# Optimization experiments

Hardware: AMD Instinct MI355X
Metric: run time of the kernel (lower is better)

The kernel has to match this reference:

```python
import jax, jax.numpy as jnp
import numpy as np
from jax import lax

S, B, IN, H, L = 256, 8192, 1, 32, 2


def setup_inputs() -> dict:
    key = jax.random.key(0)
    ks = jax.random.split(key, 12)
    s = 1.0 / np.sqrt(H)
    return {
        "x": jax.random.normal(ks[0], (S, B, IN), dtype=jnp.float32),
        "h": jax.random.normal(ks[1], (L, B, H), dtype=jnp.float32),
        "W_ih0": jax.random.uniform(ks[2], (3 * H, IN), jnp.float32, -s, s),
        "W_hh0": jax.random.uniform(ks[3], (3 * H, H), jnp.float32, -s, s),
        "b_ih0": jax.random.uniform(ks[4], (3 * H,), jnp.float32, -s, s),
        "b_hh0": jax.random.uniform(ks[5], (3 * H,), jnp.float32, -s, s),
        "W_ih1": jax.random.uniform(ks[6], (3 * H, H), jnp.float32, -s, s),
        "W_hh1": jax.random.uniform(ks[7], (3 * H, H), jnp.float32, -s, s),
        "b_ih1": jax.random.uniform(ks[8], (3 * H,), jnp.float32, -s, s),
        "b_hh1": jax.random.uniform(ks[9], (3 * H,), jnp.float32, -s, s),
        "W_out": jax.random.uniform(ks[10], (1, H), jnp.float32, -s, s),
        "b_out": jax.random.uniform(ks[11], (1,), jnp.float32, -s, s),
    }


def _gru_layer(x_seq, h0, W_ih, W_hh, b_ih, b_hh):
    # x_seq: (S, B, D_in), h0: (B, H). PyTorch GRU gate math.
    def step(h, x_t):
        gi = x_t @ W_ih.T + b_ih            # (B, 3H)
        gh = h @ W_hh.T + b_hh              # (B, 3H)
        i_r, i_z, i_n = jnp.split(gi, 3, axis=-1)
        h_r, h_z, h_n = jnp.split(gh, 3, axis=-1)
        r = jax.nn.sigmoid(i_r + h_r)
        z = jax.nn.sigmoid(i_z + h_z)
        n = jnp.tanh(i_n + r * h_n)
        h_new = (1.0 - z) * n + z * h
        return h_new, h_new

    h_last, out = lax.scan(step, h0, x_seq)
    return out, h_last


def reference(x, h, W_ih0, W_hh0, b_ih0, b_hh0, W_ih1, W_hh1, b_ih1, b_hh1, W_out, b_out):
    out0, hl0 = _gru_layer(x, h[0], W_ih0, W_hh0, b_ih0, b_hh0)
    out1, hl1 = _gru_layer(out0, h[1], W_ih1, W_hh1, b_ih1, b_hh1)
    # per-timestep Linear loop == one batched matmul over (S, B, H)
    y = out1 @ W_out.T + b_out              # (S, B, 1)
    h_state = jnp.stack([hl0, hl1], axis=0)  # (L, B, H)
    return (y, h_state)
```

## Files before the change

kernel.cpp:

```cpp
#include <hip/hip_runtime.h>


#define S_LEN 256
#define B_SZ  8192
#define H_SZ  32
#define RS    40

typedef __attribute__((ext_vector_type(8))) short short8;
typedef __attribute__((ext_vector_type(4))) float f32x4;

#define MFMA(a, b, c) __builtin_amdgcn_mfma_f32_16x16x32_bf16(a, b, c, 0, 0, 0)

__device__ __forceinline__ unsigned short bf_rne1(float f) {
    union { float f; unsigned u; } x; x.f = f;
    unsigned u = x.u + 0x7fffu + ((x.u >> 16) & 1u);
    return (unsigned short)(u >> 16);
}

#if __has_builtin(__builtin_amdgcn_cvt_pk_bf16_f32)
typedef __bf16 bf16x2 __attribute__((ext_vector_type(2)));
__device__ __forceinline__ unsigned pk2(float a, float b) {
    union { bf16x2 v; unsigned u; } c;
    c.v = __builtin_amdgcn_cvt_pk_bf16_f32(a, b);
    return c.u;
}
#else
__device__ __forceinline__ unsigned pk2(float a, float b) {
    return (unsigned)bf_rne1(a) | ((unsigned)bf_rne1(b) << 16);
}
#endif

union Frag8 { short8 s8; unsigned u[4]; };

__device__ __forceinline__ uint2 gru_combine(const f32x4& Dr, const f32x4& Dz,
                                             const f32x4& Dn, const f32x4& Dxn,
                                             float* hm) {
    float v4[4];
#pragma unroll
    for (int r = 0; r < 4; ++r) {
        const float Er = __builtin_amdgcn_exp2f(Dr[r]);
        const float rg = __builtin_amdgcn_rcpf(1.0f + Er);
        const float X  = __builtin_amdgcn_exp2f(fmaf(rg, Dn[r], Dxn[r]));
        const float Ez = __builtin_amdgcn_exp2f(Dz[r]);
        const float Nx = 1.0f + X;
        const float Nz = 1.0f + Ez;
        const float P  = Nx * Nz;
        float num = fmaf(-2.0f, Ez, P);
        num = fmaf(hm[r], Nx, num);
        const float v = num * __builtin_amdgcn_rcpf(P);
        hm[r] = v - 1.0f;
        v4[r] = v;
    }
    return make_uint2(pk2(v4[0], v4[1]), pk2(v4[2], v4[3]));
}

__global__ __launch_bounds__(256) void gru_xm(
    const float* __restrict__ x,
    const float* __restrict__ h_in,
    const float* __restrict__ W_ih0,
    const float* __restrict__ W_hh0,
    const float* __restrict__ b_ih0,
    const float* __restrict__ b_hh0,
    const float* __restrict__ W_ih1,
    const float* __restrict__ W_hh1,
    const float* __restrict__ b_ih1,
    const float* __restrict__ b_hh1,
    const float* __restrict__ W_out,
    const float* __restrict__ b_out,
    float* __restrict__ out)
{
    __shared__ __align__(16) unsigned short sh0[2][16 * RS];
    __shared__ __align__(16) unsigned short sh1[2][16 * RS];
    __shared__ __align__(16) float sx[(S_LEN + 1) * 16];
    __shared__ __align__(16) float sy[S_LEN * 16];

    const int tid  = threadIdx.x;
    const int w    = tid >> 6;
    const int lane = tid & 63;
    const int n    = lane & 15;
    const int q    = lane >> 4;
    const int base = blockIdx.x * 16;
    const int bn   = base + n;
    const int wl   = w & 1;

    for (int s = tid; s < S_LEN * 4; s += 256) {
        const int t = s >> 2, c = s & 3;
        *(float4*)&sx[t * 16 + c * 4] = *(const float4*)&x[t * B_SZ + base + c * 4];
    }

    const float SRZ = -1.4426950408889634f;
    const float SN  =  2.8853900817779268f;

    short8 A_h[3], A_i[3];
    f32x4  C_h[3], C_i3;
    short8 Awo = {0, 0, 0, 0, 0, 0, 0, 0};
    short8 Bx  = {0, 0, 0, 0, 0, 0, 0, 0};
    float  hm[4];

    if (w < 2) {
#pragma unroll
        for (int t = 0; t < 3; ++t) {
            const float sc = (t < 2) ? SRZ : SN;
            const int row = 32 * t + 16 * wl + n;
#pragma unroll
            for (int e = 0; e < 8; ++e)
                A_h[t][e] = (short)bf_rne1(W_hh0[row * H_SZ + q * 8 + e] * sc);
#pragma unroll
            for (int e = 0; e < 8; ++e)
                A_i[t][e] = (q == 0 && e == 0)
                            ? (short)bf_rne1(W_ih0[row] * sc) : (short)0;
#pragma unroll
            for (int r = 0; r < 4; ++r) {
                const int g = 32 * t + 16 * wl + 4 * q + r;
                C_h[t][r] = (t < 2) ? SRZ * (b_ih0[g] + b_hh0[g])
                                    : SN * b_hh0[g];
                if (t == 2) C_i3[r] = SN * b_ih0[g];
            }
        }
#pragma unroll
        for (int r = 0; r < 4; ++r)
            hm[r] = h_in[bn * H_SZ + 16 * wl + 4 * q + r] - 1.0f;
    } else {
#pragma unroll
        for (int t = 0; t < 3; ++t) {
            const float sc = (t < 2) ? SRZ : SN;
            const int row = 32 * t + 16 * wl + n;
#pragma unroll
            for (int e = 0; e < 8; ++e) {
                A_h[t][e] = (short)bf_rne1(W_hh1[row * H_SZ + q * 8 + e] * sc);
                A_i[t][e] = (short)bf_rne1(W_ih1[row * H_SZ + q * 8 + e] * sc);
            }
#pragma unroll
            for (int r = 0; r < 4; ++r) {
                const int g = 32 * t + 16 * wl + 4 * q + r;
                C_h[t][r] = (t < 2) ? SRZ * (b_ih1[g] + b_hh1[g])
                                    : SN * b_hh1[g];
                if (t == 2) C_i3[r] = SN * b_ih1[g];
            }
        }
#pragma unroll
        for (int r = 0; r < 4; ++r)
            hm[r] = h_in[B_SZ * H_SZ + bn * H_SZ + 16 * wl + 4 * q + r] - 1.0f;
#pragma unroll
        for (int e = 0; e < 8; ++e)
            Awo[e] = (n == 0) ? (short)bf_rne1(W_out[q * 8 + e]) : (short)0;
    }
    const f32x4 Z4 = {0.f, 0.f, 0.f, 0.f};
    const float bout = b_out[0];

    short8 B0, B1;
    {
        const float* hsrc = h_in + (size_t)(w >= 2) * B_SZ * H_SZ + bn * H_SZ + q * 8;
        Frag8 f;
        const float4 a = *(const float4*)&hsrc[0];
        const float4 b = *(const float4*)&hsrc[4];
        f.u[0] = pk2(a.x, a.y); f.u[1] = pk2(a.z, a.w);
        f.u[2] = pk2(b.x, b.y); f.u[3] = pk2(b.z, b.w);
        if (w < 2) B0 = f.s8; else B1 = f.s8;
    }

    const int wroff = n * RS + 16 * wl + 4 * q;
    const int rdoff = n * RS + 8 * q;

    __syncthreads();
    float xcur = sx[n];
    if (w < 2) __builtin_amdgcn_s_setprio(1);

    if (w < 2) {
        Frag8 bxu; bxu.s8 = Bx; bxu.u[0] = pk2(xcur, xcur); Bx = bxu.s8;
        f32x4 Dr = MFMA(A_h[0], B0, C_h[0]);  Dr = MFMA(A_i[0], Bx, Dr);
        f32x4 Dz = MFMA(A_h[1], B0, C_h[1]);  Dz = MFMA(A_i[1], Bx, Dz);
        f32x4 Dn = MFMA(A_h[2], B0, C_h[2]);
        f32x4 Dxn = MFMA(A_i[2], Bx, C_i3);
        *(uint2*)&sh0[0][wroff] = gru_combine(Dr, Dz, Dn, Dxn, hm);
        xcur = sx[16 + n];
    }
    __syncthreads();
    B0 = *(const short8*)&sh0[0][rdoff];

#pragma unroll 2
    for (int i = 1; i < S_LEN; ++i) {
        const int buf = i & 1;
        if (w < 2) {
            Frag8 bxu; bxu.s8 = Bx; bxu.u[0] = pk2(xcur, xcur); Bx = bxu.s8;
            f32x4 Dr = MFMA(A_h[0], B0, C_h[0]);  Dr = MFMA(A_i[0], Bx, Dr);
            f32x4 Dz = MFMA(A_h[1], B0, C_h[1]);  Dz = MFMA(A_i[1], Bx, Dz);
            f32x4 Dn = MFMA(A_h[2], B0, C_h[2]);
            f32x4 Dxn = MFMA(A_i[2], Bx, C_i3);
            *(uint2*)&sh0[buf][wroff] = gru_combine(Dr, Dz, Dn, Dxn, hm);
            xcur = sx[(i + 1) * 16 + n];
        } else {
            f32x4 Gr = MFMA(A_h[0], B1, C_h[0]);  Gr = MFMA(A_i[0], B0, Gr);
            f32x4 Gz = MFMA(A_h[1], B1, C_h[1]);  Gz = MFMA(A_i[1], B0, Gz);
            f32x4 Un = MFMA(A_h[2], B1, C_h[2]);
            f32x4 Vn = MFMA(A_i[2], B0, C_i3);
            *(uint2*)&sh1[buf][wroff] = gru_combine(Gr, Gz, Un, Vn, hm);
        }

        __syncthreads();

        if (w < 2) {
            B0 = *(const short8*)&sh0[buf][rdoff];
        } else {
            B0 = *(const short8*)&sh0[buf][rdoff];
            B1 = *(const short8*)&sh1[buf][rdoff];
            if (w == 2 + ((i - 1) & 1)) {
                const f32x4 yD = MFMA(Awo, B1, Z4);
                if (lane < 16) sy[(i - 1) * 16 + n] = yD[0];
            }
        }
    }

    if (w >= 2) {
        f32x4 Gr = MFMA(A_h[0], B1, C_h[0]);  Gr = MFMA(A_i[0], B0, Gr);
        f32x4 Gz = MFMA(A_h[1], B1, C_h[1]);  Gz = MFMA(A_i[1], B0, Gz);
        f32x4 Un = MFMA(A_h[2], B1, C_h[2]);
        f32x4 Vn = MFMA(A_i[2], B0, C_i3);
        *(uint2*)&sh1[0][wroff] = gru_combine(Gr, Gz, Un, Vn, hm);
    }
    __syncthreads();
    if (w == 2 + ((S_LEN - 1) & 1)) {
        B1 = *(const short8*)&sh1[0][rdoff];
        const f32x4 yD = MFMA(Awo, B1, Z4);
        if (lane < 16) sy[(S_LEN - 1) * 16 + n] = yD[0];
    }
    __syncthreads();

    for (int s = tid; s < S_LEN * 4; s += 256) {
        const int t = s >> 2, c = s & 3;
        const float4 a = *(const float4*)&sy[t * 16 + c * 4];
        *(float4*)&out[t * B_SZ + base + c * 4] =
            make_float4(a.x + bout, a.y + bout, a.z + bout, a.w + bout);
    }

    const size_t hoff = (size_t)S_LEN * B_SZ + (size_t)(w >= 2) * B_SZ * H_SZ;
    *(float4*)&out[hoff + bn * H_SZ + 16 * wl + 4 * q] =
        make_float4(hm[0] + 1.0f, hm[1] + 1.0f, hm[2] + 1.0f, hm[3] + 1.0f);
}

extern "C" void kernel_launch(void* const* d_in, const int* in_sizes, int n_in,
                              void* d_out, int out_size, void* d_ws, size_t ws_size,
                              hipStream_t stream) {
    (void)in_sizes; (void)n_in; (void)out_size; (void)d_ws; (void)ws_size;
    const float* x     = (const float*)d_in[0];
    const float* h_in  = (const float*)d_in[1];
    const float* W_ih0 = (const float*)d_in[2];
    const float* W_hh0 = (const float*)d_in[3];
    const float* b_ih0 = (const float*)d_in[4];
    const float* b_hh0 = (const float*)d_in[5];
    const float* W_ih1 = (const float*)d_in[6];
    const float* W_hh1 = (const float*)d_in[7];
    const float* b_ih1 = (const float*)d_in[8];
    const float* b_hh1 = (const float*)d_in[9];
    const float* W_out = (const float*)d_in[10];
    const float* b_out = (const float*)d_in[11];

    dim3 grid(B_SZ / 16);
    dim3 block(256);
    gru_xm<<<grid, block, 0, stream>>>(x, h_in, W_ih0, W_hh0, b_ih0, b_hh0,
                                       W_ih1, W_hh1, b_ih1, b_hh1,
                                       W_out, b_out, (float*)d_out);
}
```

Before: 231.1 us.

## Replace per-step block barriers with LDS progress-counter flags between layer waves

```diff
diff --git a/kernel.cpp b/kernel.cpp
--- a/kernel.cpp
+++ b/kernel.cpp
@@ -69,10 +69,11 @@
     const float* __restrict__ b_out,
     float* __restrict__ out)
 {
-    __shared__ __align__(16) unsigned short sh0[2][16 * RS];
+    __shared__ __align__(16) unsigned short sh0[4][16 * RS];
     __shared__ __align__(16) unsigned short sh1[2][16 * RS];
     __shared__ __align__(16) float sx[(S_LEN + 1) * 16];
     __shared__ __align__(16) float sy[S_LEN * 16];
+    __shared__ unsigned prog[4];
 
     const int tid  = threadIdx.x;
     const int w    = tid >> 6;
@@ -82,6 +83,9 @@
     const int base = blockIdx.x * 16;
     const int bn   = base + n;
     const int wl   = w & 1;
+    volatile unsigned* vp = prog;
+
+    if (tid < 4) prog[tid] = 0;
 
     for (int s = tid; s < S_LEN * 4; s += 256) {
         const int t = s >> 2, c = s & 3;
@@ -148,7 +152,7 @@
     const f32x4 Z4 = {0.f, 0.f, 0.f, 0.f};
     const float bout = b_out[0];
 
-    short8 B0, B1;
+    short8 B0i, B1i;
     {
         const float* hsrc = h_in + (size_t)(w >= 2) * B_SZ * H_SZ + bn * H_SZ + q * 8;
         Frag8 f;
@@ -156,74 +160,108 @@
         const float4 b = *(const float4*)&hsrc[4];
         f.u[0] = pk2(a.x, a.y); f.u[1] = pk2(a.z, a.w);
         f.u[2] = pk2(b.x, b.y); f.u[3] = pk2(b.z, b.w);
-        if (w < 2) B0 = f.s8; else B1 = f.s8;
+        if (w < 2) B0i = f.s8; else B1i = f.s8;
     }
 
     const int wroff = n * RS + 16 * wl + 4 * q;
     const int rdoff = n * RS + 8 * q;
 
     __syncthreads();
-    float xcur = sx[n];
-    if (w < 2) __builtin_amdgcn_s_setprio(1);
 
     if (w < 2) {
-        Frag8 bxu; bxu.s8 = Bx; bxu.u[0] = pk2(xcur, xcur); Bx = bxu.s8;
-        f32x4 Dr = MFMA(A_h[0], B0, C_h[0]);  Dr = MFMA(A_i[0], Bx, Dr);
-        f32x4 Dz = MFMA(A_h[1], B0, C_h[1]);  Dz = MFMA(A_i[1], Bx, Dz);
-        f32x4 Dn = MFMA(A_h[2], B0, C_h[2]);
-        f32x4 Dxn = MFMA(A_i[2], Bx, C_i3);
-        *(uint2*)&sh0[0][wroff] = gru_combine(Dr, Dz, Dn, Dxn, hm);
-        xcur = sx[16 + n];
-    }
-    __syncthreads();
-    B0 = *(const short8*)&sh0[0][rdoff];
-
-#pragma unroll 2
-    for (int i = 1; i < S_LEN; ++i) {
-        const int buf = i & 1;
-        if (w < 2) {
+        __builtin_amdgcn_s_setprio(1);
+        float xcur = sx[n];
+
+        {
+            Frag8 bxu; bxu.s8 = Bx; bxu.u[0] = pk2(xcur, xcur); Bx = bxu.s8;
+            f32x4 Dr = MFMA(A_h[0], B0i, C_h[0]);  Dr = MFMA(A_i[0], Bx, Dr);
+            f32x4 Dz = MFMA(A_h[1], B0i, C_h[1]);  Dz = MFMA(A_i[1], Bx, Dz);
+            f32x4 Dn = MFMA(A_h[2], B0i, C_h[2]);
+            f32x4 Dxn = MFMA(A_i[2], Bx, C_i3);
+            *(uint2*)&sh0[0][wroff] = gru_combine(Dr, Dz, Dn, Dxn, hm);
+            __threadfence_block();
+            if (lane == 0) vp[wl] = 1;
+            xcur = sx[16 + n];
+        }
+
+        for (int i = 1; i < S_LEN; ++i) {
+            const unsigned need = (i >= 3) ? (unsigned)(i - 3) : 0u;
+            for (;;) {
+                const unsigned a  = vp[1 - wl];
+                const unsigned c2 = vp[2];
+                const unsigned c3 = vp[3];
+                if (a >= (unsigned)i && c2 >= need && c3 >= need) break;
+                __builtin_amdgcn_s_sleep(1);
+            }
+            __threadfence_block();
+            const short8 B0 = *(const short8*)&sh0[(i - 1) & 3][rdoff];
             Frag8 bxu; bxu.s8 = Bx; bxu.u[0] = pk2(xcur, xcur); Bx = bxu.s8;
             f32x4 Dr = MFMA(A_h[0], B0, C_h[0]);  Dr = MFMA(A_i[0], Bx, Dr);
             f32x4 Dz = MFMA(A_h[1], B0, C_h[1]);  Dz = MFMA(A_i[1], Bx, Dz);
             f32x4 Dn = MFMA(A_h[2], B0, C_h[2]);
             f32x4 Dxn = MFMA(A_i[2], Bx, C_i3);
-            *(uint2*)&sh0[buf][wroff] = gru_combine(Dr, Dz, Dn, Dxn, hm);
+            *(uint2*)&sh0[i & 3][wroff] = gru_combine(Dr, Dz, Dn, Dxn, hm);
+            __threadfence_block();
+            if (lane == 0) vp[wl] = (unsigned)(i + 1);
             xcur = sx[(i + 1) * 16 + n];
-        } else {
+        }
+    } else {
+        short8 B1 = B1i;
+
+        {
+            for (;;) {
+                const unsigned a0 = vp[0], a1 = vp[1];
+                if (a0 >= 1u && a1 >= 1u) break;
+                __builtin_amdgcn_s_sleep(1);
+            }
+            __threadfence_block();
+            const short8 B0 = *(const short8*)&sh0[0][rdoff];
             f32x4 Gr = MFMA(A_h[0], B1, C_h[0]);  Gr = MFMA(A_i[0], B0, Gr);
             f32x4 Gz = MFMA(A_h[1], B1, C_h[1]);  Gz = MFMA(A_i[1], B0, Gz);
             f32x4 Un = MFMA(A_h[2], B1, C_h[2]);
             f32x4 Vn = MFMA(A_i[2], B0, C_i3);
-            *(uint2*)&sh1[buf][wroff] = gru_combine(Gr, Gz, Un, Vn, hm);
-        }
-
-        __syncthreads();
-
-        if (w < 2) {
-            B0 = *(const short8*)&sh0[buf][rdoff];
-        } else {
-            B0 = *(const short8*)&sh0[buf][rdoff];
-            B1 = *(const short8*)&sh1[buf][rdoff];
-            if (w == 2 + ((i - 1) & 1)) {
+            *(uint2*)&sh1[0][wroff] = gru_combine(Gr, Gz, Un, Vn, hm);
+            __threadfence_block();
+            if (lane == 0) vp[2 + wl] = 1;
+        }
+
+        for (int t = 1; t < S_LEN; ++t) {
+            for (;;) {
+                const unsigned a0 = vp[0], a1 = vp[1];
+                const unsigned pp = vp[2 + (1 - wl)];
+                if (a0 >= (unsigned)(t + 1) && a1 >= (unsigned)(t + 1) &&
+                    pp >= (unsigned)t) break;
+                __builtin_amdgcn_s_sleep(1);
+            }
+            __threadfence_block();
+            const short8 B0 = *(const short8*)&sh0[t & 3][rdoff];
+            B1 = *(const short8*)&sh1[(t - 1) & 1][rdoff];
+            if (w == 2 + ((t - 1) & 1)) {
                 const f32x4 yD = MFMA(Awo, B1, Z4);
-                if (lane < 16) sy[(i - 1) * 16 + n] = yD[0];
-            }
-        }
-    }
-
-    if (w >= 2) {
-        f32x4 Gr = MFMA(A_h[0], B1, C_h[0]);  Gr = MFMA(A_i[0], B0, Gr);
-        f32x4 Gz = MFMA(A_h[1], B1, C_h[1]);  Gz = MFMA(A_i[1], B0, Gz);
-        f32x4 Un = MFMA(A_h[2], B1, C_h[2]);
-        f32x4 Vn = MFMA(A_i[2], B0, C_i3);
-        *(uint2*)&sh1[0][wroff] = gru_combine(Gr, Gz, Un, Vn, hm);
-    }
-    __syncthreads();
-    if (w == 2 + ((S_LEN - 1) & 1)) {
-        B1 = *(const short8*)&sh1[0][rdoff];
-        const f32x4 yD = MFMA(Awo, B1, Z4);
-        if (lane < 16) sy[(S_LEN - 1) * 16 + n] = yD[0];
-    }
+                if (lane < 16) sy[(t - 1) * 16 + n] = yD[0];
+            }
+            f32x4 Gr = MFMA(A_h[0], B1, C_h[0]);  Gr = MFMA(A_i[0], B0, Gr);
+            f32x4 Gz = MFMA(A_h[1], B1, C_h[1]);  Gz = MFMA(A_i[1], B0, Gz);
+            f32x4 Un = MFMA(A_h[2], B1, C_h[2]);
+            f32x4 Vn = MFMA(A_i[2], B0, C_i3);
+            *(uint2*)&sh1[t & 1][wroff] = gru_combine(Gr, Gz, Un, Vn, hm);
+            __threadfence_block();
+            if (lane == 0) vp[2 + wl] = (unsigned)(t + 1);
+        }
+
+        if (w == 2 + ((S_LEN - 1) & 1)) {
+            for (;;) {
+                const unsigned pp = vp[2 + (1 - wl)];
+                if (pp >= (unsigned)S_LEN) break;
+                __builtin_amdgcn_s_sleep(1);
+            }
+            __threadfence_block();
+            B1 = *(const short8*)&sh1[(S_LEN - 1) & 1][rdoff];
+            const f32x4 yD = MFMA(Awo, B1, Z4);
+            if (lane < 16) sy[(S_LEN - 1) * 16 + n] = yD[0];
+        }
+    }
+
     __syncthreads();
 
     for (int s = tid; s < S_LEN * 4; s += 256) {
```

Measured after the change: 246.6 us. 6.7% more time.
